# Kernel optimization log

Hardware: AMD Instinct MI355X
Metric: run time of the kernel (lower is better)

The kernel has to match this reference:

```python
import jax, jax.numpy as jnp
import numpy as np

N_USERS, N_ITEMS, D, F = 100000, 50000, 64, 768
N_NODES = N_USERS + N_ITEMS
N_EDGES = 4800000
BATCH = 4096
LN_EPS = 1e-5
CONTENT_LOSS_W = 0.1


def _layernorm(x):
    # default nn.LayerNorm: weight=1, bias=0
    m = jnp.mean(x, axis=-1, keepdims=True)
    v = jnp.mean(jnp.square(x - m), axis=-1, keepdims=True)
    return (x - m) * jax.lax.rsqrt(v + LN_EPS)


def setup_inputs() -> dict:
    key = jax.random.key(0)
    ks = jax.random.split(key, 12)
    return {
        "users": jax.random.randint(ks[0], (BATCH,), 0, N_USERS),
        "pos_items": jax.random.randint(ks[1], (BATCH,), 0, N_ITEMS),
        "neg_items": jax.random.randint(ks[2], (BATCH,), 0, N_ITEMS),
        "edge_src": jax.random.randint(ks[3], (N_EDGES,), 0, N_NODES, dtype=jnp.int32),
        "edge_dst": jax.random.randint(ks[4], (N_EDGES,), 0, N_NODES, dtype=jnp.int32),
        # symmetric-normalized adjacency values are ~1/deg
        "edge_weight": jax.random.uniform(ks[5], (N_EDGES,), jnp.float32) / 32.0,
        "user_emb": jax.random.normal(ks[6], (N_USERS, D), jnp.float32) * 0.1,
        "item_emb": jax.random.normal(ks[7], (N_ITEMS, D), jnp.float32) * 0.1,
        "content_features": jax.random.normal(ks[8], (N_ITEMS, F), jnp.float32),
        "W_proj": jax.random.normal(ks[9], (F, D), jnp.float32) * 0.02,
        "b_proj": jnp.zeros((D,), jnp.float32),
        "w_gate": jax.random.normal(ks[10], (F,), jnp.float32) * 0.02,
        "b_gate": jnp.zeros((1,), jnp.float32),
        "n_layers": 3,
    }


def reference(users, pos_items, neg_items, edge_src, edge_dst, edge_weight,
              user_emb, item_emb, content_features, W_proj, b_proj,
              w_gate, b_gate, n_layers):
    # gated fusion of collaborative and content item embeddings
    items_content = content_features @ W_proj + b_proj           # [I, D]
    gate = jax.nn.sigmoid(content_features @ w_gate + b_gate)    # [I]
    gate = gate[:, None]
    items = (1.0 - gate) * item_emb + gate * items_content       # [I, D]

    all_emb = jnp.concatenate([user_emb, items], axis=0)          # [N, D]
    acc = all_emb
    emb = all_emb
    for _ in range(n_layers):
        # SpMM: out[dst] += w * emb[src]
        agg = jax.ops.segment_sum(edge_weight[:, None] * emb[edge_src],
                                  edge_dst, num_segments=N_NODES)
        emb = _layernorm(agg) + emb   # LayerNorm + residual
        acc = acc + emb
    light_out = acc / (n_layers + 1)                              # mean over layers

    final_users, final_items = light_out[:N_USERS], light_out[N_USERS:]
    users_out = final_users[users]
    pos_out = final_items[pos_items]
    neg_out = final_items[neg_items]
    content_loss = jnp.mean(jnp.square(final_items - items_content)) * CONTENT_LOSS_W
    return users_out, pos_out, neg_out, content_loss
```

## Files before the change

### kernel.cpp

```cpp
#include <hip/hip_runtime.h>
#include <hip/hip_bf16.h>

#define N_USERS 100000
#define N_ITEMS 50000
#define N_NODES 150000
#define DD 64
#define FF 768
#define N_EDGES_C 4800000
#define BATCH 4096
#define LN_EPS 1e-5f
#define CONTENT_LOSS_W 0.1f

#define SCAN_BLK 1024
#define SCAN_NBLK 147

#define NBUCK 147
#define BIN_TILE 4096

#define KWIN 24

typedef __attribute__((ext_vector_type(8))) short short8;
typedef __attribute__((ext_vector_type(4))) float f32x4;

__device__ inline float b2f(unsigned short v) {
    union { unsigned int i; float f; } u;
    u.i = ((unsigned int)v) << 16;
    return u.f;
}
__device__ inline unsigned short f2b(float f) {
    union { float f; unsigned int i; } u; u.f = f;
    unsigned int r = u.i + 0x7fff + ((u.i >> 16) & 1);
    return (unsigned short)(r >> 16);
}
__device__ inline short bfc(float f) {
    __hip_bfloat16 h = __float2bfloat16(f);
    return *reinterpret_cast<short*>(&h);
}

__global__ __launch_bounds__(256) void init_users_k(
    const float* __restrict__ ue, unsigned short* __restrict__ emb)
{
    int gid = blockIdx.x * 256 + threadIdx.x;
    size_t base = (size_t)gid * 4;
    float4 v = *reinterpret_cast<const float4*>(ue + base);
    ushort4 o;
    o.x = f2b(v.x); o.y = f2b(v.y); o.z = f2b(v.z); o.w = f2b(v.w);
    *reinterpret_cast<ushort4*>(emb + base) = o;
}

__global__ __launch_bounds__(256) void wp_stage_k(
    const float* __restrict__ Wp, unsigned short* __restrict__ bstg)
{
    int tid = blockIdx.x * 256 + threadIdx.x;
    int e    = tid & 7;
    int lane = (tid >> 3) & 63;
    int nt   = (tid >> 9) & 3;
    int kw   = tid >> 11;
    int k = kw * 32 + ((lane >> 4) << 3) + e;
    int n = nt * 16 + (lane & 15);
    bstg[tid] = (unsigned short)bfc(Wp[k * DD + n]);
}

__global__ __launch_bounds__(256) void content_mfma_k(
    const float* __restrict__ cf, const unsigned short* __restrict__ bstg,
    const float* __restrict__ bp, const float* __restrict__ wg,
    const float* __restrict__ bg, const float* __restrict__ item_emb,
    float* __restrict__ items_content,
    unsigned short* __restrict__ emb, float* __restrict__ acc_items)
{
    const int wt = blockIdx.x * 4 + (threadIdx.x >> 6);
    if (wt >= N_ITEMS / 16) return;
    const int lane = threadIdx.x & 63;
    const int row0 = wt * 16;

    const int lrow = lane & 15;
    const int kgrp = lane >> 4;

    const float* aptr = cf + (size_t)(row0 + lrow) * FF + (kgrp << 3);
    const float* wptr = wg + (kgrp << 3);
    const short8* bptr = reinterpret_cast<const short8*>(bstg) + lane;

    f32x4 acc0 = {0.f, 0.f, 0.f, 0.f};
    f32x4 acc1 = {0.f, 0.f, 0.f, 0.f};
    f32x4 acc2 = {0.f, 0.f, 0.f, 0.f};
    f32x4 acc3 = {0.f, 0.f, 0.f, 0.f};
    float gp = 0.f;

    #pragma unroll 4
    for (int kw = 0; kw < KWIN; ++kw) {
        float4 a0 = *reinterpret_cast<const float4*>(aptr + kw * 32);
        float4 a1 = *reinterpret_cast<const float4*>(aptr + kw * 32 + 4);
        float4 w0 = *reinterpret_cast<const float4*>(wptr + kw * 32);
        float4 w1 = *reinterpret_cast<const float4*>(wptr + kw * 32 + 4);

        gp += a0.x * w0.x + a0.y * w0.y + a0.z * w0.z + a0.w * w0.w;
        gp += a1.x * w1.x + a1.y * w1.y + a1.z * w1.z + a1.w * w1.w;

        short8 af;
        af[0] = bfc(a0.x); af[1] = bfc(a0.y); af[2] = bfc(a0.z); af[3] = bfc(a0.w);
        af[4] = bfc(a1.x); af[5] = bfc(a1.y); af[6] = bfc(a1.z); af[7] = bfc(a1.w);

        const short8* bb = bptr + (size_t)kw * 256;
        short8 b0 = bb[0];
        short8 b1 = bb[64];
        short8 b2 = bb[128];
        short8 b3 = bb[192];

        acc0 = __builtin_amdgcn_mfma_f32_16x16x32_bf16(af, b0, acc0, 0, 0, 0);
        acc1 = __builtin_amdgcn_mfma_f32_16x16x32_bf16(af, b1, acc1, 0, 0, 0);
        acc2 = __builtin_amdgcn_mfma_f32_16x16x32_bf16(af, b2, acc2, 0, 0, 0);
        acc3 = __builtin_amdgcn_mfma_f32_16x16x32_bf16(af, b3, acc3, 0, 0, 0);
    }

    gp += __shfl_xor(gp, 16);
    gp += __shfl_xor(gp, 32);
    const float g = 1.f / (1.f + __expf(-(gp + bg[0])));

    const int rbase = kgrp << 2;
    f32x4 accs[4] = {acc0, acc1, acc2, acc3};
    #pragma unroll
    for (int nt = 0; nt < 4; ++nt) {
        const int col = nt * 16 + lrow;
        const float bpv = bp[col];
        #pragma unroll
        for (int r = 0; r < 4; ++r) {
            const int rit = rbase + r;
            const int row = row0 + rit;
            const float ic = accs[nt][r] + bpv;
            const float gr = __shfl(g, rit);
            const size_t o = (size_t)row * DD + col;
            const float it = (1.f - gr) * item_emb[o] + gr * ic;
            items_content[o] = ic;
            emb[(size_t)(N_USERS + row) * DD + col] = f2b(it);
            acc_items[o] = it;
        }
    }
}

__global__ __launch_bounds__(256) void hist_k(
    const int* __restrict__ ed, int* __restrict__ cursor)
{
    int t = blockIdx.x * 256 + threadIdx.x;
    if (t < N_EDGES_C / 4) {
        int4 d = reinterpret_cast<const int4*>(ed)[t];
        atomicAdd(&cursor[d.x], 1);
        atomicAdd(&cursor[d.y], 1);
        atomicAdd(&cursor[d.z], 1);
        atomicAdd(&cursor[d.w], 1);
    }
}

__global__ __launch_bounds__(SCAN_BLK) void scan_blocksum_k(
    const int* __restrict__ cursor, int* __restrict__ partials)
{
    __shared__ int sdata[SCAN_BLK];
    int i = blockIdx.x * SCAN_BLK + threadIdx.x;
    int v = (i < N_NODES) ? cursor[i] : 0;
    sdata[threadIdx.x] = v;
    __syncthreads();
    for (int off = SCAN_BLK / 2; off; off >>= 1) {
        if (threadIdx.x < off) sdata[threadIdx.x] += sdata[threadIdx.x + off];
        __syncthreads();
    }
    if (threadIdx.x == 0) partials[blockIdx.x] = sdata[0];
}

__global__ __launch_bounds__(256) void scan_partials_k(int* __restrict__ partials)
{
    __shared__ int sdata[256];
    int t = threadIdx.x;
    int v = (t < SCAN_NBLK) ? partials[t] : 0;
    sdata[t] = v;
    __syncthreads();
    for (int off = 1; off < 256; off <<= 1) {
        int x = (t >= off) ? sdata[t - off] : 0;
        __syncthreads();
        sdata[t] += x;
        __syncthreads();
    }
    if (t < SCAN_NBLK) partials[t] = sdata[t] - v;
}

__global__ __launch_bounds__(SCAN_BLK) void scan_write_k(
    const int* __restrict__ partials, int* __restrict__ cursor)
{
    __shared__ int sdata[SCAN_BLK];
    int i = blockIdx.x * SCAN_BLK + threadIdx.x;
    int t = threadIdx.x;
    int v = (i < N_NODES) ? cursor[i] : 0;
    sdata[t] = v;
    __syncthreads();
    for (int off = 1; off < SCAN_BLK; off <<= 1) {
        int x = (t >= off) ? sdata[t - off] : 0;
        __syncthreads();
        sdata[t] += x;
        __syncthreads();
    }
    if (i < N_NODES)
        cursor[i] = partials[blockIdx.x] + sdata[t] - v;
}

__global__ __launch_bounds__(256) void bucket_init_k(
    const int* __restrict__ cursor, int* __restrict__ bucket_cursor)
{
    int t = threadIdx.x;
    if (t < NBUCK) bucket_cursor[t] = cursor[t << 10];
}

__global__ __launch_bounds__(256) void bin_k(
    const int* __restrict__ ed, const int* __restrict__ es,
    const float* __restrict__ ew, int* __restrict__ bucket_cursor,
    uint2* __restrict__ binned)
{
    __shared__ uint2 stage[BIN_TILE];
    __shared__ int h[NBUCK];
    __shared__ int o[NBUCK];
    __shared__ int gbase[NBUCK];
    __shared__ int scanbuf[256];

    const int t = threadIdx.x;
    const int base = blockIdx.x * BIN_TILE;
    const int cnt = min(BIN_TILE, N_EDGES_C - base);

    for (int i = t; i < NBUCK; i += 256) h[i] = 0;
    __syncthreads();

    int ld[16]; int ls[16]; float lw[16]; int lb[16];
    #pragma unroll
    for (int k = 0; k < 16; ++k) {
        int i = t + k * 256;
        if (i < cnt) {
            int d = ed[base + i];
            ld[k] = d;
            ls[k] = es[base + i];
            lw[k] = ew[base + i];
            int b = d >> 10;
            lb[k] = b;
            atomicAdd(&h[b], 1);
        } else lb[k] = -1;
    }
    __syncthreads();

    {
        int v = (t < NBUCK) ? h[t] : 0;
        scanbuf[t] = v;
        __syncthreads();
        for (int off = 1; off < 256; off <<= 1) {
            int x = (t >= off) ? scanbuf[t - off] : 0;
            __syncthreads();
            scanbuf[t] += x;
            __syncthreads();
        }
        if (t < NBUCK) o[t] = scanbuf[t] - v;
    }
    __syncthreads();

    if (t < NBUCK) h[t] = o[t];
    __syncthreads();

    #pragma unroll
    for (int k = 0; k < 16; ++k) {
        if (lb[k] >= 0) {
            int p = atomicAdd(&h[lb[k]], 1);
            unsigned key = ((unsigned)ls[k] << 10) | (unsigned)(ld[k] & 1023);
            stage[p] = make_uint2(key, __float_as_uint(lw[k]));
        }
    }
    __syncthreads();

    if (t < NBUCK) {
        int c = h[t] - o[t];
        gbase[t] = (c > 0) ? atomicAdd(&bucket_cursor[t], c) : 0;
    }
    __syncthreads();

    for (int i = t; i < cnt; i += 256) {
        int lo = 0, hi = NBUCK - 1;
        while (lo < hi) {
            int mid = (lo + hi + 1) >> 1;
            if (o[mid] <= i) lo = mid; else hi = mid - 1;
        }
        binned[gbase[lo] + (i - o[lo])] = stage[i];
    }
}

__global__ __launch_bounds__(256) void scatter_k(
    const uint2* __restrict__ binned, const int* __restrict__ cursor,
    uint2* __restrict__ adj)
{
    __shared__ int lc[1024];
    const int b = blockIdx.x;
    const int t = threadIdx.x;
    const int nb = b << 10;
    for (int j = t; j < 1024; j += 256) {
        int n = nb + j;
        lc[j] = (n < N_NODES) ? cursor[n] : 0;
    }
    __syncthreads();
    const int s0 = cursor[nb];
    const int s1 = (b == NBUCK - 1) ? N_EDGES_C : cursor[nb + 1024];
    for (int i = s0 + t; i < s1; i += 256) {
        uint2 e = binned[i];
        int ln = (int)(e.x & 1023u);
        unsigned src = e.x >> 10;
        int p = atomicAdd(&lc[ln], 1);
        adj[p] = make_uint2(src, e.y);
    }
}

__global__ __launch_bounds__(256) void agg_ln_k(
    const unsigned short* __restrict__ emb_in,
    unsigned short* __restrict__ emb_out,
    float* __restrict__ acc_items,
    const int* __restrict__ cursor, const uint2* __restrict__ adj)
{
    const int n = blockIdx.x * 4 + (threadIdx.x >> 6);
    const int lane = threadIdx.x & 63;
    const int g = lane >> 4;
    const int q = lane & 15;
    const int qo = q << 2;

    const int beg = cursor[n];
    const int end = (n == N_NODES - 1) ? N_EDGES_C : cursor[n + 1];

    float a0 = 0.f, a1 = 0.f, a2 = 0.f, a3 = 0.f;

    int j = beg;
    for (; j + 15 < end; j += 16) {
        uint2 e0 = adj[j + g];
        uint2 e1 = adj[j + 4 + g];
        uint2 e2 = adj[j + 8 + g];
        uint2 e3 = adj[j + 12 + g];
        ushort4 r0 = *reinterpret_cast<const ushort4*>(emb_in + (size_t)e0.x * DD + qo);
        ushort4 r1 = *reinterpret_cast<const ushort4*>(emb_in + (size_t)e1.x * DD + qo);
        ushort4 r2 = *reinterpret_cast<const ushort4*>(emb_in + (size_t)e2.x * DD + qo);
        ushort4 r3 = *reinterpret_cast<const ushort4*>(emb_in + (size_t)e3.x * DD + qo);
        float w0 = __uint_as_float(e0.y), w1 = __uint_as_float(e1.y);
        float w2 = __uint_as_float(e2.y), w3 = __uint_as_float(e3.y);
        a0 += w0 * b2f(r0.x); a1 += w0 * b2f(r0.y); a2 += w0 * b2f(r0.z); a3 += w0 * b2f(r0.w);
        a0 += w1 * b2f(r1.x); a1 += w1 * b2f(r1.y); a2 += w1 * b2f(r1.z); a3 += w1 * b2f(r1.w);
        a0 += w2 * b2f(r2.x); a1 += w2 * b2f(r2.y); a2 += w2 * b2f(r2.z); a3 += w2 * b2f(r2.w);
        a0 += w3 * b2f(r3.x); a1 += w3 * b2f(r3.y); a2 += w3 * b2f(r3.z); a3 += w3 * b2f(r3.w);
    }
    for (; j + 3 < end; j += 4) {
        uint2 e = adj[j + g];
        ushort4 r = *reinterpret_cast<const ushort4*>(emb_in + (size_t)e.x * DD + qo);
        float w = __uint_as_float(e.y);
        a0 += w * b2f(r.x); a1 += w * b2f(r.y); a2 += w * b2f(r.z); a3 += w * b2f(r.w);
    }
    if (g < end - j) {
        uint2 e = adj[j + g];
        ushort4 r = *reinterpret_cast<const ushort4*>(emb_in + (size_t)e.x * DD + qo);
        float w = __uint_as_float(e.y);
        a0 += w * b2f(r.x); a1 += w * b2f(r.y); a2 += w * b2f(r.z); a3 += w * b2f(r.w);
    }

    a0 += __shfl_xor(a0, 16); a0 += __shfl_xor(a0, 32);
    a1 += __shfl_xor(a1, 16); a1 += __shfl_xor(a1, 32);
    a2 += __shfl_xor(a2, 16); a2 += __shfl_xor(a2, 32);
    a3 += __shfl_xor(a3, 16); a3 += __shfl_xor(a3, 32);

    float s = a0 + a1 + a2 + a3;
    s += __shfl_xor(s, 1); s += __shfl_xor(s, 2);
    s += __shfl_xor(s, 4); s += __shfl_xor(s, 8);
    const float m = s * (1.f / 64.f);
    const float d0 = a0 - m, d1 = a1 - m, d2 = a2 - m, d3 = a3 - m;
    float vv = d0 * d0 + d1 * d1 + d2 * d2 + d3 * d3;
    vv += __shfl_xor(vv, 1); vv += __shfl_xor(vv, 2);
    vv += __shfl_xor(vv, 4); vv += __shfl_xor(vv, 8);
    const float rstd = rsqrtf(vv * (1.f / 64.f) + LN_EPS);

    if (g == 0) {
        const size_t o = (size_t)n * DD + qo;
        ushort4 own = *reinterpret_cast<const ushort4*>(emb_in + o);
        float e0 = d0 * rstd + b2f(own.x);
        float e1 = d1 * rstd + b2f(own.y);
        float e2 = d2 * rstd + b2f(own.z);
        float e3 = d3 * rstd + b2f(own.w);
        ushort4 ob;
        ob.x = f2b(e0); ob.y = f2b(e1); ob.z = f2b(e2); ob.w = f2b(e3);
        *reinterpret_cast<ushort4*>(emb_out + o) = ob;
        if (n >= N_USERS) {
            float4* ap = reinterpret_cast<float4*>(
                acc_items + (size_t)(n - N_USERS) * DD + qo);
            float4 v = *ap;
            v.x += e0; v.y += e1; v.z += e2; v.w += e3;
            *ap = v;
        }
    }
}

__global__ __launch_bounds__(256) void gather_acc_k(
    const int* __restrict__ users, const int* __restrict__ pos,
    const int* __restrict__ neg, const unsigned short* __restrict__ emb_state,
    float* __restrict__ out, int init)
{
    int gid = blockIdx.x * 256 + threadIdx.x;
    int part = gid / (BATCH * DD);
    int r = gid - part * (BATCH * DD);
    int b = r >> 6, c = r & 63;
    int node;
    if (part == 0)      node = users[b];
    else if (part == 1) node = N_USERS + pos[b];
    else                node = N_USERS + neg[b];
    float v = b2f(emb_state[(size_t)node * DD + c]);
    if (init) out[gid] = v;
    else      out[gid] += v;
}

__global__ __launch_bounds__(256) void loss_k(
    const float* __restrict__ acc_items, const float* __restrict__ ic,
    float* __restrict__ loss_slot)
{
    const int total = N_ITEMS * DD;
    int stride = gridDim.x * 256;
    float p = 0.f;
    for (int i = blockIdx.x * 256 + threadIdx.x; i < total; i += stride) {
        float d = acc_items[i] * 0.25f - ic[i];
        p += d * d;
    }
    #pragma unroll
    for (int off = 32; off; off >>= 1) p += __shfl_xor(p, off);
    __shared__ float red[4];
    if ((threadIdx.x & 63) == 0) red[threadIdx.x >> 6] = p;
    __syncthreads();
    if (threadIdx.x == 0)
        atomicAdd(loss_slot, red[0] + red[1] + red[2] + red[3]);
}

__global__ __launch_bounds__(256) void final_out_k(
    const float* __restrict__ loss_slot, float* __restrict__ out)
{
    int gid = blockIdx.x * 256 + threadIdx.x;
    out[gid] *= 0.25f;
    if (gid == 0)
        out[3 * BATCH * DD] =
            loss_slot[0] * (CONTENT_LOSS_W / (float)(N_ITEMS * DD));
}

extern "C" void kernel_launch(void* const* d_in, const int* in_sizes, int n_in,
                              void* d_out, int out_size, void* d_ws, size_t ws_size,
                              hipStream_t stream)
{
    const int* users = (const int*)d_in[0];
    const int* pos   = (const int*)d_in[1];
    const int* neg   = (const int*)d_in[2];
    const int* es    = (const int*)d_in[3];
    const int* ed    = (const int*)d_in[4];
    const float* ew  = (const float*)d_in[5];
    const float* ue  = (const float*)d_in[6];
    const float* ie  = (const float*)d_in[7];
    const float* cf  = (const float*)d_in[8];
    const float* Wp  = (const float*)d_in[9];
    const float* bp  = (const float*)d_in[10];
    const float* wg  = (const float*)d_in[11];
    const float* bg  = (const float*)d_in[12];
    float* out = (float*)d_out;

    unsigned short* embA = (unsigned short*)d_ws;
    unsigned short* embB = embA + (size_t)N_NODES * DD;
    float* acc_items = (float*)(embB + (size_t)N_NODES * DD);
    float* ic        = acc_items + (size_t)N_ITEMS * DD;
    float* loss_slot = ic + (size_t)N_ITEMS * DD;
    int*   cursor    = (int*)(loss_slot + 16);
    int*   partials  = cursor + 150016;
    int*   bucket_cursor = partials + 256;
    uint2* adj       = (uint2*)(bucket_cursor + 256);
    uint2* binned    = (uint2*)embB;
    unsigned short* bstg = embA;

    hipMemsetAsync(cursor, 0, 150016 * sizeof(int), stream);
    hipMemsetAsync(loss_slot, 0, sizeof(float), stream);

    hist_k<<<(N_EDGES_C / 4 + 255) / 256, 256, 0, stream>>>(ed, cursor);
    scan_blocksum_k<<<SCAN_NBLK, SCAN_BLK, 0, stream>>>(cursor, partials);
    scan_partials_k<<<1, 256, 0, stream>>>(partials);
    scan_write_k<<<SCAN_NBLK, SCAN_BLK, 0, stream>>>(partials, cursor);
    bucket_init_k<<<1, 256, 0, stream>>>(cursor, bucket_cursor);
    bin_k<<<(N_EDGES_C + BIN_TILE - 1) / BIN_TILE, 256, 0, stream>>>(
        ed, es, ew, bucket_cursor, binned);
    scatter_k<<<NBUCK, 256, 0, stream>>>(binned, cursor, adj);

    wp_stage_k<<<192, 256, 0, stream>>>(Wp, bstg);
    content_mfma_k<<<(N_ITEMS / 16 + 3) / 4, 256, 0, stream>>>(
        cf, bstg, bp, wg, bg, ie, ic, embA, acc_items);
    init_users_k<<<(N_USERS * DD / 4) / 256, 256, 0, stream>>>(ue, embA);
    gather_acc_k<<<3 * BATCH * DD / 256, 256, 0, stream>>>(users, pos, neg,
                                                           embA, out, 1);

    unsigned short* cur = embA;
    unsigned short* nxt = embB;
    for (int l = 0; l < 3; ++l) {
        agg_ln_k<<<N_NODES / 4, 256, 0, stream>>>(cur, nxt, acc_items,
                                                  cursor, adj);
        gather_acc_k<<<3 * BATCH * DD / 256, 256, 0, stream>>>(users, pos, neg,
                                                               nxt, out, 0);
        unsigned short* t = cur; cur = nxt; nxt = t;
    }

    loss_k<<<2048, 256, 0, stream>>>(acc_items, ic, loss_slot);
    final_out_k<<<3 * BATCH * DD / 256, 256, 0, stream>>>(loss_slot, out);
}
```

Before: 1.004 ms.

## Replace per-node global histogram and scan with bucket-level histogram and in-scatter scan

The CSR build no longer does 4.8M global atomics on a per-node counter array followed by a three-kernel scan. It now counts edges per 1024-node bucket using shared-memory atomics, scans the 147 bucket counts, and computes per-node offsets inside the scatter kernel through a block-local histogram and scan. This removes global atomic contention and several kernel launches. In exchange, scatter_k reads the binned edges twice and runs 1024-thread blocks, which gives only 147 blocks of parallelism.

```diff
diff --git a/kernel.cpp b/kernel.cpp
--- a/kernel.cpp
+++ b/kernel.cpp
@@ -11,11 +11,9 @@
 #define LN_EPS 1e-5f
 #define CONTENT_LOSS_W 0.1f
 
-#define SCAN_BLK 1024
-#define SCAN_NBLK 147
-
 #define NBUCK 147
 #define BIN_TILE 4096
+#define HIST_BLKS 1200
 
 #define KWIN 24
 
@@ -137,39 +135,34 @@
     }
 }
 
-__global__ __launch_bounds__(256) void hist_k(
-    const int* __restrict__ ed, int* __restrict__ cursor)
-{
-    int t = blockIdx.x * 256 + threadIdx.x;
-    if (t < N_EDGES_C / 4) {
+__global__ __launch_bounds__(256) void bucket_hist_k(
+    const int* __restrict__ ed, int* __restrict__ bucket_cnt)
+{
+    __shared__ int lh[NBUCK];
+    for (int i = threadIdx.x; i < NBUCK; i += 256) lh[i] = 0;
+    __syncthreads();
+    const int stride = HIST_BLKS * 256;
+    for (int t = blockIdx.x * 256 + threadIdx.x; t < N_EDGES_C / 4; t += stride) {
         int4 d = reinterpret_cast<const int4*>(ed)[t];
-        atomicAdd(&cursor[d.x], 1);
-        atomicAdd(&cursor[d.y], 1);
-        atomicAdd(&cursor[d.z], 1);
-        atomicAdd(&cursor[d.w], 1);
-    }
-}
-
-__global__ __launch_bounds__(SCAN_BLK) void scan_blocksum_k(
-    const int* __restrict__ cursor, int* __restrict__ partials)
-{
-    __shared__ int sdata[SCAN_BLK];
-    int i = blockIdx.x * SCAN_BLK + threadIdx.x;
-    int v = (i < N_NODES) ? cursor[i] : 0;
-    sdata[threadIdx.x] = v;
-    __syncthreads();
-    for (int off = SCAN_BLK / 2; off; off >>= 1) {
-        if (threadIdx.x < off) sdata[threadIdx.x] += sdata[threadIdx.x + off];
-        __syncthreads();
-    }
-    if (threadIdx.x == 0) partials[blockIdx.x] = sdata[0];
-}
-
-__global__ __launch_bounds__(256) void scan_partials_k(int* __restrict__ partials)
+        atomicAdd(&lh[d.x >> 10], 1);
+        atomicAdd(&lh[d.y >> 10], 1);
+        atomicAdd(&lh[d.z >> 10], 1);
+        atomicAdd(&lh[d.w >> 10], 1);
+    }
+    __syncthreads();
+    for (int i = threadIdx.x; i < NBUCK; i += 256) {
+        int c = lh[i];
+        if (c) atomicAdd(&bucket_cnt[i], c);
+    }
+}
+
+__global__ __launch_bounds__(256) void bucket_scan_k(
+    const int* __restrict__ bucket_cnt, int* __restrict__ bucket_base,
+    int* __restrict__ bucket_cursor)
 {
     __shared__ int sdata[256];
     int t = threadIdx.x;
-    int v = (t < SCAN_NBLK) ? partials[t] : 0;
+    int v = (t < NBUCK) ? bucket_cnt[t] : 0;
     sdata[t] = v;
     __syncthreads();
     for (int off = 1; off < 256; off <<= 1) {
@@ -178,33 +171,12 @@
         sdata[t] += x;
         __syncthreads();
     }
-    if (t < SCAN_NBLK) partials[t] = sdata[t] - v;
-}
-
-__global__ __launch_bounds__(SCAN_BLK) void scan_write_k(
-    const int* __restrict__ partials, int* __restrict__ cursor)
-{
-    __shared__ int sdata[SCAN_BLK];
-    int i = blockIdx.x * SCAN_BLK + threadIdx.x;
-    int t = threadIdx.x;
-    int v = (i < N_NODES) ? cursor[i] : 0;
-    sdata[t] = v;
-    __syncthreads();
-    for (int off = 1; off < SCAN_BLK; off <<= 1) {
-        int x = (t >= off) ? sdata[t - off] : 0;
-        __syncthreads();
-        sdata[t] += x;
-        __syncthreads();
-    }
-    if (i < N_NODES)
-        cursor[i] = partials[blockIdx.x] + sdata[t] - v;
-}
-
-__global__ __launch_bounds__(256) void bucket_init_k(
-    const int* __restrict__ cursor, int* __restrict__ bucket_cursor)
-{
-    int t = threadIdx.x;
-    if (t < NBUCK) bucket_cursor[t] = cursor[t << 10];
+    if (t < NBUCK) {
+        int b = sdata[t] - v;
+        bucket_base[t] = b;
+        bucket_cursor[t] = b;
+    }
+    if (t == NBUCK - 1) bucket_base[NBUCK] = sdata[t];
 }
 
 __global__ __launch_bounds__(256) void bin_k(
@@ -284,27 +256,43 @@
     }
 }
 
-__global__ __launch_bounds__(256) void scatter_k(
-    const uint2* __restrict__ binned, const int* __restrict__ cursor,
-    uint2* __restrict__ adj)
-{
-    __shared__ int lc[1024];
+__global__ __launch_bounds__(1024) void scatter_k(
+    const uint2* __restrict__ binned, const int* __restrict__ bucket_base,
+    int* __restrict__ cursor, uint2* __restrict__ adj)
+{
+    __shared__ int lh[1024];
+    __shared__ int sdata[1024];
     const int b = blockIdx.x;
     const int t = threadIdx.x;
     const int nb = b << 10;
-    for (int j = t; j < 1024; j += 256) {
-        int n = nb + j;
-        lc[j] = (n < N_NODES) ? cursor[n] : 0;
-    }
-    __syncthreads();
-    const int s0 = cursor[nb];
-    const int s1 = (b == NBUCK - 1) ? N_EDGES_C : cursor[nb + 1024];
-    for (int i = s0 + t; i < s1; i += 256) {
+    const int s0 = bucket_base[b];
+    const int s1 = bucket_base[b + 1];
+
+    lh[t] = 0;
+    __syncthreads();
+    for (int i = s0 + t; i < s1; i += 1024)
+        atomicAdd(&lh[binned[i].x & 1023u], 1);
+    __syncthreads();
+
+    int v = lh[t];
+    sdata[t] = v;
+    __syncthreads();
+    for (int off = 1; off < 1024; off <<= 1) {
+        int x = (t >= off) ? sdata[t - off] : 0;
+        __syncthreads();
+        sdata[t] += x;
+        __syncthreads();
+    }
+    const int start = s0 + sdata[t] - v;
+    if (nb + t < N_NODES) cursor[nb + t] = start;
+    lh[t] = start;
+    __syncthreads();
+
+    for (int i = s0 + t; i < s1; i += 1024) {
         uint2 e = binned[i];
         int ln = (int)(e.x & 1023u);
-        unsigned src = e.x >> 10;
-        int p = atomicAdd(&lc[ln], 1);
-        adj[p] = make_uint2(src, e.y);
+        int p = atomicAdd(&lh[ln], 1);
+        adj[p] = make_uint2(e.x >> 10, e.y);
     }
 }
 
@@ -463,23 +451,21 @@
     float* ic        = acc_items + (size_t)N_ITEMS * DD;
     float* loss_slot = ic + (size_t)N_ITEMS * DD;
     int*   cursor    = (int*)(loss_slot + 16);
-    int*   partials  = cursor + 150016;
-    int*   bucket_cursor = partials + 256;
+    int*   bucket_cnt    = cursor + 150016;
+    int*   bucket_base   = bucket_cnt + 256;
+    int*   bucket_cursor = bucket_base + 256;
     uint2* adj       = (uint2*)(bucket_cursor + 256);
     uint2* binned    = (uint2*)embB;
     unsigned short* bstg = embA;
 
-    hipMemsetAsync(cursor, 0, 150016 * sizeof(int), stream);
+    hipMemsetAsync(bucket_cnt, 0, 256 * sizeof(int), stream);
     hipMemsetAsync(loss_slot, 0, sizeof(float), stream);
 
-    hist_k<<<(N_EDGES_C / 4 + 255) / 256, 256, 0, stream>>>(ed, cursor);
-    scan_blocksum_k<<<SCAN_NBLK, SCAN_BLK, 0, stream>>>(cursor, partials);
-    scan_partials_k<<<1, 256, 0, stream>>>(partials);
-    scan_write_k<<<SCAN_NBLK, SCAN_BLK, 0, stream>>>(partials, cursor);
-    bucket_init_k<<<1, 256, 0, stream>>>(cursor, bucket_cursor);
+    bucket_hist_k<<<HIST_BLKS, 256, 0, stream>>>(ed, bucket_cnt);
+    bucket_scan_k<<<1, 256, 0, stream>>>(bucket_cnt, bucket_base, bucket_cursor);
     bin_k<<<(N_EDGES_C + BIN_TILE - 1) / BIN_TILE, 256, 0, stream>>>(
         ed, es, ew, bucket_cursor, binned);
-    scatter_k<<<NBUCK, 256, 0, stream>>>(binned, cursor, adj);
+    scatter_k<<<NBUCK, 1024, 0, stream>>>(binned, bucket_base, cursor, adj);
 
     wp_stage_k<<<192, 256, 0, stream>>>(Wp, bstg);
     content_mfma_k<<<(N_ITEMS / 16 + 3) / 4, 256, 0, stream>>>(
```

After: 838.8 us. 1.2x faster.
